# Kernel tuning notes

Measured on AMD Instinct MI355X. Metric: run time of the kernel, lower is better.

## Reference

```python
import jax, jax.numpy as jnp
import numpy as np

HEAD_DIM = 64
N_HEADS = 32
N_KV = 8
ROPE_BASE = 500000.0
FREQ_CONFIG = {"factor": 32.0, "low_freq_factor": 1.0, "high_freq_factor": 4.0, "original_context_length": 8192}


def _rope_tables(head_dim, theta, n_pos, fc):
    # faithful to precompute_rope_params with llama3 freq scaling
    inv_freq = 1.0 / theta ** (np.arange(0, head_dim, 2, dtype=np.float32) / head_dim)
    low_wl = fc["original_context_length"] / fc["low_freq_factor"]
    high_wl = fc["original_context_length"] / fc["high_freq_factor"]
    wavelen = 2.0 * np.pi / inv_freq
    inv_l = np.where(wavelen > low_wl, inv_freq / fc["factor"], inv_freq)
    smooth = (fc["original_context_length"] / wavelen - fc["low_freq_factor"]) / (fc["high_freq_factor"] - fc["low_freq_factor"])
    smoothed = (1.0 - smooth) * (inv_freq / fc["factor"]) + smooth * inv_freq
    med = (wavelen <= low_wl) & (wavelen >= high_wl)
    inv_freq = np.where(med, smoothed, inv_l)
    pos = np.arange(n_pos, dtype=np.float32)
    angles = pos[:, None] * inv_freq[None, :]          # [T, head_dim/2]
    angles = np.concatenate([angles, angles], axis=1)  # [T, head_dim]
    return jnp.asarray(np.cos(angles), jnp.float32), jnp.asarray(np.sin(angles), jnp.float32)


def _apply_rope(x, cos, sin):
    # x: [b, h, t, d]; cos/sin: [t, d]
    d = x.shape[-1]
    x1, x2 = x[..., : d // 2], x[..., d // 2:]
    rotated = jnp.concatenate([-x2, x1], axis=-1)
    return x * cos[None, None] + rotated * sin[None, None]


def setup_inputs() -> dict:
    key = jax.random.key(0)
    ks = jax.random.split(key, 5)
    b, t, d = 1, 2048, 2048
    s = 0.02
    return {
        "x": jax.random.normal(ks[0], (b, t, d), jnp.float32),
        "Wq": jax.random.normal(ks[1], (d, d), jnp.float32) * s,
        "Wk": jax.random.normal(ks[2], (N_KV * HEAD_DIM, d), jnp.float32) * s,
        "Wv": jax.random.normal(ks[3], (N_KV * HEAD_DIM, d), jnp.float32) * s,
        "Wo": jax.random.normal(ks[4], (d, d), jnp.float32) * s,
        "start_pos": 0,
    }


def reference(x, Wq, Wk, Wv, Wo, start_pos):
    b, t, _ = x.shape
    cos, sin = _rope_tables(HEAD_DIM, ROPE_BASE, start_pos + t, FREQ_CONFIG)
    cos, sin = cos[start_pos:start_pos + t], sin[start_pos:start_pos + t]

    q = (x @ Wq.T).reshape(b, t, N_HEADS, HEAD_DIM).transpose(0, 2, 1, 3)  # [b,H,t,d]
    k = (x @ Wk.T).reshape(b, t, N_KV, HEAD_DIM).transpose(0, 2, 1, 3)     # [b,G,t,d]
    v = (x @ Wv.T).reshape(b, t, N_KV, HEAD_DIM).transpose(0, 2, 1, 3)

    q = _apply_rope(q, cos, sin)
    k = _apply_rope(k, cos, sin)

    n_rep = N_HEADS // N_KV
    k = jnp.repeat(k, n_rep, axis=1)  # [b,H,t,d]
    v = jnp.repeat(v, n_rep, axis=1)

    scores = jnp.einsum("bhqd,bhkd->bhqk", q, k)
    causal = jnp.triu(jnp.ones((t, t), bool), k=1)
    scores = jnp.where(causal[None, None], -jnp.inf, scores) / jnp.sqrt(jnp.float32(HEAD_DIM))
    weights = jax.nn.softmax(scores, axis=-1)
    ctx = jnp.einsum("bhqk,bhkd->bhqd", weights, v)
    ctx = ctx.transpose(0, 2, 1, 3).reshape(b, t, N_HEADS * HEAD_DIM)
    return ctx @ Wo.T
```

## Files before the change

kernel.cpp:

```cpp
#include <hip/hip_runtime.h>
#include <math.h>

#define T_SEQ 2048
#define D_MODEL 2048
#define HEAD_DIM 64
#define N_HEADS 32
#define N_KV 8

using short8 = __attribute__((ext_vector_type(8))) short;
using f32x4  = __attribute__((ext_vector_type(4))) float;

#define MFMA16(a, b, c) __builtin_amdgcn_mfma_f32_16x16x32_bf16(a, b, c, 0, 0, 0)

__device__ __forceinline__ unsigned short f2bf(float f) {
    unsigned int u = __builtin_bit_cast(unsigned int, f);
    u += 0x7fff + ((u >> 16) & 1);
    return (unsigned short)(u >> 16);
}
__device__ __forceinline__ float bf2f(unsigned short h) {
    unsigned int u = ((unsigned int)h) << 16;
    return __builtin_bit_cast(float, u);
}
__device__ __forceinline__ void gld_lds16(const ushort* g, ushort* l) {
    __builtin_amdgcn_global_load_lds((const __attribute__((address_space(1))) void*)g,
                                     (__attribute__((address_space(3))) void*)l, 16, 0, 0);
}

__global__ void rope_tables_kernel(float* __restrict__ cosT, float* __restrict__ sinT,
                                   const int* __restrict__ start_pos, int T) {
    int t = blockIdx.x;
    int i = threadIdx.x;
    float pos = (float)(start_pos[0] + t);
    float expo = (float)i / 32.0f;
    float inv_freq = 1.0f / powf(500000.0f, expo);
    const float two_pi = 6.283185307179586f;
    float wavelen = two_pi / inv_freq;
    const float low_wl = 8192.0f;
    const float high_wl = 2048.0f;
    float inv;
    if (wavelen > low_wl) {
        inv = inv_freq / 32.0f;
    } else if (wavelen < high_wl) {
        inv = inv_freq;
    } else {
        float smooth = (8192.0f / wavelen - 1.0f) / 3.0f;
        inv = (1.0f - smooth) * (inv_freq / 32.0f) + smooth * inv_freq;
    }
    float ang = pos * inv;
    cosT[i * T + t] = cosf(ang);
    sinT[i * T + t] = sinf(ang);
}

__global__ __launch_bounds__(256) void cast_all_kernel(
    const float* __restrict__ x, const float* __restrict__ wq,
    const float* __restrict__ wk, const float* __restrict__ wv,
    const float* __restrict__ wo,
    ushort* __restrict__ xb, ushort* __restrict__ wqb,
    ushort* __restrict__ wkb, ushort* __restrict__ wvb, ushort* __restrict__ wob) {
    int i = blockIdx.x * 256 + threadIdx.x;
    const float* src; ushort* dst; int off;
    if (i < 1048576)      { src = x;  dst = xb;  off = i; }
    else if (i < 2097152) { src = wq; dst = wqb; off = i - 1048576; }
    else if (i < 2359296) { src = wk; dst = wkb; off = i - 2097152; }
    else if (i < 2621440) { src = wv; dst = wvb; off = i - 2359296; }
    else                  { src = wo; dst = wob; off = i - 2621440; }
    float4 v = ((const float4*)src)[off];
    ushort4 o;
    o.x = f2bf(v.x); o.y = f2bf(v.y); o.z = f2bf(v.z); o.w = f2bf(v.w);
    ((ushort4*)dst)[off] = o;
}

__global__ __launch_bounds__(256) void gemm_qkv(
    const ushort* __restrict__ X, const ushort* __restrict__ Wqb,
    const ushort* __restrict__ Wkb, const ushort* __restrict__ Wvb,
    ushort* __restrict__ Qo, ushort* __restrict__ Ko, ushort* __restrict__ Vto,
    const float* __restrict__ cosT, const float* __restrict__ sinT,
    int T, int D) {
    __shared__ __align__(16) ushort As[2][2048];
    __shared__ __align__(16) ushort Bs[2][4096];
    const int tid = threadIdx.x;
    const int w = tid >> 6, l = tid & 63;
    const int m0 = blockIdx.x * 64;
    const int n0g = blockIdx.y * 128;

    const ushort* B;
    ushort* Cout;
    int n0, doRope;
    if (n0g < 2048)      { B = Wqb + (size_t)n0g * D;          Cout = Qo;  n0 = n0g;        doRope = 1; }
    else if (n0g < 2560) { B = Wkb + (size_t)(n0g - 2048) * D; Cout = Ko;  n0 = n0g - 2048; doRope = 1; }
    else                 { B = Wvb + (size_t)(n0g - 2560) * D; Cout = Vto; n0 = n0g - 2560; doRope = 0; }

    const int wm = (w >> 1) * 32, wn = (w & 1) * 64;
    const int lr = l & 15;
    const int quad = l >> 4;

    f32x4 zero = {0.f, 0.f, 0.f, 0.f};
    f32x4 acc[2][4];
#pragma unroll
    for (int i = 0; i < 2; ++i)
#pragma unroll
        for (int j = 0; j < 4; ++j) acc[i][j] = zero;

    const int srow = l >> 2;
    const int scg  = ((l & 3) ^ (srow & 3)) * 8;
    const ushort* Ag0 = X + (size_t)(m0 + 16 * w + srow) * D + scg;
    const ushort* Bg0 = B + (size_t)(16 * (2 * w) + srow) * D + scg;
    const ushort* Bg1 = B + (size_t)(16 * (2 * w + 1) + srow) * D + scg;

    gld_lds16(Ag0, &As[0][w * 512]);
    gld_lds16(Bg0, &Bs[0][(2 * w) * 512]);
    gld_lds16(Bg1, &Bs[0][(2 * w + 1) * 512]);

    const int rsw = (quad ^ (lr & 3)) * 8;
    for (int k0 = 0; k0 < D; k0 += 32) {
        const int b = (k0 >> 5) & 1;
        __syncthreads();
        if (k0 + 32 < D) {
            gld_lds16(Ag0 + k0 + 32, &As[b ^ 1][w * 512]);
            gld_lds16(Bg0 + k0 + 32, &Bs[b ^ 1][(2 * w) * 512]);
            gld_lds16(Bg1 + k0 + 32, &Bs[b ^ 1][(2 * w + 1) * 512]);
        }
        short8 af[2], bf[4];
#pragma unroll
        for (int i = 0; i < 2; ++i) af[i] = *(const short8*)&As[b][(wm + i * 16 + lr) * 32 + rsw];
#pragma unroll
        for (int j = 0; j < 4; ++j) bf[j] = *(const short8*)&Bs[b][(wn + j * 16 + lr) * 32 + rsw];
#pragma unroll
        for (int i = 0; i < 2; ++i)
#pragma unroll
            for (int j = 0; j < 4; ++j)
                acc[i][j] = MFMA16(af[i], bf[j], acc[i][j]);
    }

    const int mbase = m0 + wm + quad * 4;
    if (doRope) {
#pragma unroll
        for (int i = 0; i < 2; ++i) {
            int trow = mbase + i * 16;
#pragma unroll
            for (int j = 0; j < 2; ++j) {
                int i1 = lr + j * 16;
                float4 c4 = *(const float4*)&cosT[(size_t)i1 * T + trow];
                float4 s4 = *(const float4*)&sinT[(size_t)i1 * T + trow];
                int n1 = n0 + wn + lr + j * 16;
                int n2 = n1 + 32;
                size_t b1 = (size_t)(n1 >> 6) * ((size_t)T * 64) + (size_t)(n1 & 63);
                size_t b2 = (size_t)(n2 >> 6) * ((size_t)T * 64) + (size_t)(n2 & 63);
                float cs[4] = {c4.x, c4.y, c4.z, c4.w};
                float sn[4] = {s4.x, s4.y, s4.z, s4.w};
#pragma unroll
                for (int r = 0; r < 4; ++r) {
                    float x1 = acc[i][j][r], x2 = acc[i][j + 2][r];
                    Cout[b1 + (size_t)(trow + r) * 64] = f2bf(x1 * cs[r] - x2 * sn[r]);
                    Cout[b2 + (size_t)(trow + r) * 64] = f2bf(x2 * cs[r] + x1 * sn[r]);
                }
            }
        }
    } else {
#pragma unroll
        for (int i = 0; i < 2; ++i)
#pragma unroll
            for (int j = 0; j < 4; ++j) {
                int n = n0 + wn + lr + j * 16;
                int m = mbase + i * 16;
                ushort4 o;
                o.x = f2bf(acc[i][j][0]); o.y = f2bf(acc[i][j][1]);
                o.z = f2bf(acc[i][j][2]); o.w = f2bf(acc[i][j][3]);
                *(ushort4*)&Vto[(size_t)n * T + m] = o;
            }
    }
}

__global__ __launch_bounds__(256) void gemm_bt_f32(const ushort* __restrict__ A,
                                                   const ushort* __restrict__ B,
                                                   float* __restrict__ C,
                                                   int M, int N, int K) {
    __shared__ __align__(16) ushort As[2][2048];
    __shared__ __align__(16) ushort Bs[2][4096];
    const int tid = threadIdx.x;
    const int w = tid >> 6, l = tid & 63;
    const int m0 = blockIdx.x * 64, n0 = blockIdx.y * 128;
    const int wm = (w >> 1) * 32, wn = (w & 1) * 64;
    const int lr = l & 15;
    const int quad = l >> 4;

    f32x4 zero = {0.f, 0.f, 0.f, 0.f};
    f32x4 acc[2][4];
#pragma unroll
    for (int i = 0; i < 2; ++i)
#pragma unroll
        for (int j = 0; j < 4; ++j) acc[i][j] = zero;

    const int srow = l >> 2;
    const int scg  = ((l & 3) ^ (srow & 3)) * 8;
    const ushort* Ag0 = A + (size_t)(m0 + 16 * w + srow) * K + scg;
    const ushort* Bg0 = B + (size_t)(n0 + 16 * (2 * w) + srow) * K + scg;
    const ushort* Bg1 = B + (size_t)(n0 + 16 * (2 * w + 1) + srow) * K + scg;

    gld_lds16(Ag0, &As[0][w * 512]);
    gld_lds16(Bg0, &Bs[0][(2 * w) * 512]);
    gld_lds16(Bg1, &Bs[0][(2 * w + 1) * 512]);

    const int rsw = (quad ^ (lr & 3)) * 8;
    for (int k0 = 0; k0 < K; k0 += 32) {
        const int b = (k0 >> 5) & 1;
        __syncthreads();
        if (k0 + 32 < K) {
            gld_lds16(Ag0 + k0 + 32, &As[b ^ 1][w * 512]);
            gld_lds16(Bg0 + k0 + 32, &Bs[b ^ 1][(2 * w) * 512]);
            gld_lds16(Bg1 + k0 + 32, &Bs[b ^ 1][(2 * w + 1) * 512]);
        }
        short8 af[2], bf[4];
#pragma unroll
        for (int i = 0; i < 2; ++i) af[i] = *(const short8*)&As[b][(wm + i * 16 + lr) * 32 + rsw];
#pragma unroll
        for (int j = 0; j < 4; ++j) bf[j] = *(const short8*)&Bs[b][(wn + j * 16 + lr) * 32 + rsw];
#pragma unroll
        for (int i = 0; i < 2; ++i)
#pragma unroll
            for (int j = 0; j < 4; ++j)
                acc[i][j] = MFMA16(af[i], bf[j], acc[i][j]);
    }

    const int mbase = m0 + wm + quad * 4;
    const int nbase = n0 + wn + lr;
#pragma unroll
    for (int i = 0; i < 2; ++i)
#pragma unroll
        for (int j = 0; j < 4; ++j)
#pragma unroll
            for (int r = 0; r < 4; ++r)
                C[(size_t)(mbase + i * 16 + r) * N + (nbase + j * 16)] = acc[i][j][r];
}

__global__ __launch_bounds__(256) void attn_mfma(const ushort* __restrict__ Q,
                                                 const ushort* __restrict__ K,
                                                 const ushort* __restrict__ Vt,
                                                 ushort* __restrict__ ctx, int T) {
    __shared__ __align__(16) ushort Ks[2][4096];
    __shared__ __align__(16) ushort Vs[2][4096];
    __shared__ __align__(16) ushort Ps[4][2304];
    const int tid = threadIdx.x, w = tid >> 6, l = tid & 63;
    const int lr = l & 15, quad = l >> 4;
    const int h = blockIdx.y, hk = h >> 2;
    const ushort* Kb = K + (size_t)hk * T * 64;
    const ushort* Vb = Vt + (size_t)hk * 64 * T;

    const int srow = l >> 3;
    const int sc   = ((l & 7) ^ srow) * 8;
    const int si0 = 2 * w, si1 = 2 * w + 1;
    const int swz = (lr & 7);
    f32x4 zero = {0.f, 0.f, 0.f, 0.f};

    for (int phase = 0; phase < 2; ++phase) {
        const int qt = phase == 0 ? (15 - (int)blockIdx.x) : (int)blockIdx.x;
        const int qbase = qt * 128;

        short8 qf[2][2];
#pragma unroll
        for (int ni = 0; ni < 2; ++ni)
#pragma unroll
            for (int ks = 0; ks < 2; ++ks)
                qf[ni][ks] = *(const short8*)(Q + ((size_t)h * T + qbase + w * 32 + ni * 16 + lr) * 64 + ks * 32 + quad * 8);

        f32x4 oacc[2][4];
#pragma unroll
        for (int ni = 0; ni < 2; ++ni)
#pragma unroll
            for (int dj = 0; dj < 4; ++dj) oacc[ni][dj] = zero;
        float lsum[2] = {0.f, 0.f};

        const int ntiles = 2 * qt + 2;
        const int diag = 2 * qt + (w >> 1);
        const int qrow0 = qbase + w * 32 + lr;

        gld_lds16(Kb + (size_t)(8 * si0 + srow) * 64 + sc, &Ks[0][si0 * 512]);
        gld_lds16(Kb + (size_t)(8 * si1 + srow) * 64 + sc, &Ks[0][si1 * 512]);
        gld_lds16(Vb + (size_t)(8 * si0 + srow) * T + sc, &Vs[0][si0 * 512]);
        gld_lds16(Vb + (size_t)(8 * si1 + srow) * T + sc, &Vs[0][si1 * 512]);

        for (int kt = 0; kt < ntiles; ++kt) {
            const int b = kt & 1;
            __syncthreads();
            if (kt + 1 < ntiles) {
                const int k0n = (kt + 1) * 64;
                gld_lds16(Kb + (size_t)(k0n + 8 * si0 + srow) * 64 + sc, &Ks[b ^ 1][si0 * 512]);
                gld_lds16(Kb + (size_t)(k0n + 8 * si1 + srow) * 64 + sc, &Ks[b ^ 1][si1 * 512]);
                gld_lds16(Vb + (size_t)(8 * si0 + srow) * T + k0n + sc, &Vs[b ^ 1][si0 * 512]);
                gld_lds16(Vb + (size_t)(8 * si1 + srow) * T + k0n + sc, &Vs[b ^ 1][si1 * 512]);
            }
            if (kt > diag) continue;
            const int k0 = kt * 64;

            f32x4 s[4][2];
#pragma unroll
            for (int mi = 0; mi < 4; ++mi)
#pragma unroll
                for (int ni = 0; ni < 2; ++ni) s[mi][ni] = zero;
#pragma unroll
            for (int ks = 0; ks < 2; ++ks)
#pragma unroll
                for (int mi = 0; mi < 4; ++mi) {
                    short8 kf = *(const short8*)&Ks[b][(mi * 16 + lr) * 64 + ((4 * ks + quad) ^ swz) * 8];
                    s[mi][0] = MFMA16(kf, qf[0][ks], s[mi][0]);
                    s[mi][1] = MFMA16(kf, qf[1][ks], s[mi][1]);
                }

            const bool masked = (kt == diag);
#pragma unroll
            for (int mi = 0; mi < 4; ++mi)
#pragma unroll
                for (int ni = 0; ni < 2; ++ni) {
                    float pv[4];
#pragma unroll
                    for (int r = 0; r < 4; ++r) {
                        float p = __expf(s[mi][ni][r] * 0.125f);
                        if (masked && (k0 + mi * 16 + quad * 4 + r > qrow0 + ni * 16)) p = 0.f;
                        lsum[ni] += p;
                        pv[r] = p;
                    }
                    ushort4 pk;
                    pk.x = f2bf(pv[0]); pk.y = f2bf(pv[1]); pk.z = f2bf(pv[2]); pk.w = f2bf(pv[3]);
                    *(ushort4*)&Ps[w][(ni * 16 + lr) * 72 + mi * 16 + quad * 4] = pk;
                }

#pragma unroll
            for (int ks2 = 0; ks2 < 2; ++ks2) {
                short8 pf0 = *(const short8*)&Ps[w][lr * 72 + ks2 * 32 + quad * 8];
                short8 pf1 = *(const short8*)&Ps[w][(16 + lr) * 72 + ks2 * 32 + quad * 8];
#pragma unroll
                for (int dj = 0; dj < 4; ++dj) {
                    short8 vf = *(const short8*)&Vs[b][(dj * 16 + lr) * 64 + ((4 * ks2 + quad) ^ swz) * 8];
                    oacc[0][dj] = MFMA16(pf0, vf, oacc[0][dj]);
                    oacc[1][dj] = MFMA16(pf1, vf, oacc[1][dj]);
                }
            }
        }

        float inv[2][4];
#pragma unroll
        for (int ni = 0; ni < 2; ++ni) {
            float v = lsum[ni];
            v += __shfl_xor(v, 16, 64);
            v += __shfl_xor(v, 32, 64);
#pragma unroll
            for (int r = 0; r < 4; ++r)
                inv[ni][r] = 1.f / __shfl(v, quad * 4 + r, 64);
        }

#pragma unroll
        for (int ni = 0; ni < 2; ++ni)
#pragma unroll
            for (int dj = 0; dj < 4; ++dj) {
                int col = h * 64 + dj * 16 + lr;
#pragma unroll
                for (int r = 0; r < 4; ++r) {
                    int row = qbase + w * 32 + ni * 16 + quad * 4 + r;
                    ctx[(size_t)row * 2048 + col] = f2bf(oacc[ni][dj][r] * inv[ni][r]);
                }
            }
    }
}

extern "C" void kernel_launch(void* const* d_in, const int* in_sizes, int n_in,
                              void* d_out, int out_size, void* d_ws, size_t ws_size,
                              hipStream_t stream) {
    const float* x  = (const float*)d_in[0];
    const float* Wq = (const float*)d_in[1];
    const float* Wk = (const float*)d_in[2];
    const float* Wv = (const float*)d_in[3];
    const float* Wo = (const float*)d_in[4];
    const int* start_pos = (const int*)d_in[5];
    float* out = (float*)d_out;

    const int T = T_SEQ, D = D_MODEL;
    const int KV = N_KV * HEAD_DIM;

    char* w = (char*)d_ws;
    float* cosT = (float*)w;            w += (size_t)32 * T * 4;
    float* sinT = (float*)w;            w += (size_t)32 * T * 4;
    ushort* xbf  = (ushort*)w;          w += (size_t)T * D * 2;
    ushort* wqbf = (ushort*)w;          w += (size_t)D * D * 2;
    ushort* wkbf = (ushort*)w;          w += (size_t)KV * D * 2;
    ushort* wvbf = (ushort*)w;          w += (size_t)KV * D * 2;
    ushort* wobf = (ushort*)w;          w += (size_t)D * D * 2;
    ushort* qbf  = (ushort*)w;          w += (size_t)N_HEADS * T * 64 * 2;
    ushort* kbf  = (ushort*)w;          w += (size_t)N_KV * T * 64 * 2;
    ushort* vtbf = (ushort*)w;          w += (size_t)N_KV * 64 * T * 2;
    ushort* ctxbf = xbf;

    rope_tables_kernel<<<dim3(T), dim3(32), 0, stream>>>(cosT, sinT, start_pos, T);

    cast_all_kernel<<<dim3(14336), dim3(256), 0, stream>>>(x, Wq, Wk, Wv, Wo,
                                                           xbf, wqbf, wkbf, wvbf, wobf);

    gemm_qkv<<<dim3(T / 64, (D + 2 * KV) / 128), dim3(256), 0, stream>>>(
        xbf, wqbf, wkbf, wvbf, qbf, kbf, vtbf, cosT, sinT, T, D);

    attn_mfma<<<dim3(8, N_HEADS), dim3(256), 0, stream>>>(qbf, kbf, vtbf, ctxbf, T);

    gemm_bt_f32<<<dim3(T / 64, D / 128), dim3(256), 0, stream>>>(ctxbf, wobf, out, T, D, D);
}
```

Before: 251.5 us.

## Split attention key range across two warp groups and deepen GEMM K-stage

The attention kernel now runs 512 threads per block. Two groups of four warps each process alternate 64-key tiles for the same query rows, and their partial outputs and row sums are merged through shared memory at the end of each phase. Both GEMM kernels now stage 64 K-columns per iteration instead of 32, which halves the number of barriers and loop trips. The cost is more shared memory per block, an extra merge step with added barriers, and possible loss of occupancy.

Result: faster. 218.6 us (-13.1%).

```diff
diff --git a/kernel.cpp b/kernel.cpp
--- a/kernel.cpp
+++ b/kernel.cpp
@@ -16,10 +16,6 @@
     unsigned int u = __builtin_bit_cast(unsigned int, f);
     u += 0x7fff + ((u >> 16) & 1);
     return (unsigned short)(u >> 16);
-}
-__device__ __forceinline__ float bf2f(unsigned short h) {
-    unsigned int u = ((unsigned int)h) << 16;
-    return __builtin_bit_cast(float, u);
 }
 __device__ __forceinline__ void gld_lds16(const ushort* g, ushort* l) {
     __builtin_amdgcn_global_load_lds((const __attribute__((address_space(1))) void*)g,
@@ -76,8 +72,8 @@
     ushort* __restrict__ Qo, ushort* __restrict__ Ko, ushort* __restrict__ Vto,
     const float* __restrict__ cosT, const float* __restrict__ sinT,
     int T, int D) {
-    __shared__ __align__(16) ushort As[2][2048];
-    __shared__ __align__(16) ushort Bs[2][4096];
+    __shared__ __align__(16) ushort As[2][2][2048];
+    __shared__ __align__(16) ushort Bs[2][2][4096];
     const int tid = threadIdx.x;
     const int w = tid >> 6, l = tid & 63;
     const int m0 = blockIdx.x * 64;
@@ -103,34 +99,40 @@
 
     const int srow = l >> 2;
     const int scg  = ((l & 3) ^ (srow & 3)) * 8;
-    const ushort* Ag0 = X + (size_t)(m0 + 16 * w + srow) * D + scg;
+    const ushort* Ag  = X + (size_t)(m0 + 16 * w + srow) * D + scg;
     const ushort* Bg0 = B + (size_t)(16 * (2 * w) + srow) * D + scg;
     const ushort* Bg1 = B + (size_t)(16 * (2 * w + 1) + srow) * D + scg;
 
-    gld_lds16(Ag0, &As[0][w * 512]);
-    gld_lds16(Bg0, &Bs[0][(2 * w) * 512]);
-    gld_lds16(Bg1, &Bs[0][(2 * w + 1) * 512]);
+#define GSTAGE(k0v, nb) { \
+    gld_lds16(Ag  + (k0v),      &As[nb][0][w * 512]); \
+    gld_lds16(Ag  + (k0v) + 32, &As[nb][1][w * 512]); \
+    gld_lds16(Bg0 + (k0v),      &Bs[nb][0][(2 * w) * 512]); \
+    gld_lds16(Bg0 + (k0v) + 32, &Bs[nb][1][(2 * w) * 512]); \
+    gld_lds16(Bg1 + (k0v),      &Bs[nb][0][(2 * w + 1) * 512]); \
+    gld_lds16(Bg1 + (k0v) + 32, &Bs[nb][1][(2 * w + 1) * 512]); }
+
+    GSTAGE(0, 0);
 
     const int rsw = (quad ^ (lr & 3)) * 8;
-    for (int k0 = 0; k0 < D; k0 += 32) {
-        const int b = (k0 >> 5) & 1;
+    for (int k0 = 0; k0 < D; k0 += 64) {
+        const int b = (k0 >> 6) & 1;
         __syncthreads();
-        if (k0 + 32 < D) {
-            gld_lds16(Ag0 + k0 + 32, &As[b ^ 1][w * 512]);
-            gld_lds16(Bg0 + k0 + 32, &Bs[b ^ 1][(2 * w) * 512]);
-            gld_lds16(Bg1 + k0 + 32, &Bs[b ^ 1][(2 * w + 1) * 512]);
-        }
-        short8 af[2], bf[4];
-#pragma unroll
-        for (int i = 0; i < 2; ++i) af[i] = *(const short8*)&As[b][(wm + i * 16 + lr) * 32 + rsw];
-#pragma unroll
-        for (int j = 0; j < 4; ++j) bf[j] = *(const short8*)&Bs[b][(wn + j * 16 + lr) * 32 + rsw];
-#pragma unroll
-        for (int i = 0; i < 2; ++i)
-#pragma unroll
-            for (int j = 0; j < 4; ++j)
-                acc[i][j] = MFMA16(af[i], bf[j], acc[i][j]);
+        if (k0 + 64 < D) GSTAGE(k0 + 64, b ^ 1);
+#pragma unroll
+        for (int sub = 0; sub < 2; ++sub) {
+            short8 af[2], bf[4];
+#pragma unroll
+            for (int i = 0; i < 2; ++i) af[i] = *(const short8*)&As[b][sub][(wm + i * 16 + lr) * 32 + rsw];
+#pragma unroll
+            for (int j = 0; j < 4; ++j) bf[j] = *(const short8*)&Bs[b][sub][(wn + j * 16 + lr) * 32 + rsw];
+#pragma unroll
+            for (int i = 0; i < 2; ++i)
+#pragma unroll
+                for (int j = 0; j < 4; ++j)
+                    acc[i][j] = MFMA16(af[i], bf[j], acc[i][j]);
+        }
     }
+#undef GSTAGE
 
     const int mbase = m0 + wm + quad * 4;
     if (doRope) {
@@ -175,8 +177,8 @@
                                                    const ushort* __restrict__ B,
                                                    float* __restrict__ C,
                                                    int M, int N, int K) {
-    __shared__ __align__(16) ushort As[2][2048];
-    __shared__ __align__(16) ushort Bs[2][4096];
+    __shared__ __align__(16) ushort As[2][2][2048];
+    __shared__ __align__(16) ushort Bs[2][2][4096];
     const int tid = threadIdx.x;
     const int w = tid >> 6, l = tid & 63;
     const int m0 = blockIdx.x * 64, n0 = blockIdx.y * 128;
@@ -193,34 +195,40 @@
 
     const int srow = l >> 2;
     const int scg  = ((l & 3) ^ (srow & 3)) * 8;
-    const ushort* Ag0 = A + (size_t)(m0 + 16 * w + srow) * K + scg;
+    const ushort* Ag  = A + (size_t)(m0 + 16 * w + srow) * K + scg;
     const ushort* Bg0 = B + (size_t)(n0 + 16 * (2 * w) + srow) * K + scg;
     const ushort* Bg1 = B + (size_t)(n0 + 16 * (2 * w + 1) + srow) * K + scg;
 
-    gld_lds16(Ag0, &As[0][w * 512]);
-    gld_lds16(Bg0, &Bs[0][(2 * w) * 512]);
-    gld_lds16(Bg1, &Bs[0][(2 * w + 1) * 512]);
+#define GSTAGE(k0v, nb) { \
+    gld_lds16(Ag  + (k0v),      &As[nb][0][w * 512]); \
+    gld_lds16(Ag  + (k0v) + 32, &As[nb][1][w * 512]); \
+    gld_lds16(Bg0 + (k0v),      &Bs[nb][0][(2 * w) * 512]); \
+    gld_lds16(Bg0 + (k0v) + 32, &Bs[nb][1][(2 * w) * 512]); \
+    gld_lds16(Bg1 + (k0v),      &Bs[nb][0][(2 * w + 1) * 512]); \
+    gld_lds16(Bg1 + (k0v) + 32, &Bs[nb][1][(2 * w + 1) * 512]); }
+
+    GSTAGE(0, 0);
 
     const int rsw = (quad ^ (lr & 3)) * 8;
-    for (int k0 = 0; k0 < K; k0 += 32) {
-        const int b = (k0 >> 5) & 1;
+    for (int k0 = 0; k0 < K; k0 += 64) {
+        const int b = (k0 >> 6) & 1;
         __syncthreads();
-        if (k0 + 32 < K) {
-            gld_lds16(Ag0 + k0 + 32, &As[b ^ 1][w * 512]);
-            gld_lds16(Bg0 + k0 + 32, &Bs[b ^ 1][(2 * w) * 512]);
-            gld_lds16(Bg1 + k0 + 32, &Bs[b ^ 1][(2 * w + 1) * 512]);
-        }
-        short8 af[2], bf[4];
-#pragma unroll
-        for (int i = 0; i < 2; ++i) af[i] = *(const short8*)&As[b][(wm + i * 16 + lr) * 32 + rsw];
-#pragma unroll
-        for (int j = 0; j < 4; ++j) bf[j] = *(const short8*)&Bs[b][(wn + j * 16 + lr) * 32 + rsw];
-#pragma unroll
-        for (int i = 0; i < 2; ++i)
-#pragma unroll
-            for (int j = 0; j < 4; ++j)
-                acc[i][j] = MFMA16(af[i], bf[j], acc[i][j]);
+        if (k0 + 64 < K) GSTAGE(k0 + 64, b ^ 1);
+#pragma unroll
+        for (int sub = 0; sub < 2; ++sub) {
+            short8 af[2], bf[4];
+#pragma unroll
+            for (int i = 0; i < 2; ++i) af[i] = *(const short8*)&As[b][sub][(wm + i * 16 + lr) * 32 + rsw];
+#pragma unroll
+            for (int j = 0; j < 4; ++j) bf[j] = *(const short8*)&Bs[b][sub][(wn + j * 16 + lr) * 32 + rsw];
+#pragma unroll
+            for (int i = 0; i < 2; ++i)
+#pragma unroll
+                for (int j = 0; j < 4; ++j)
+                    acc[i][j] = MFMA16(af[i], bf[j], acc[i][j]);
+        }
     }
+#undef GSTAGE
 
     const int mbase = m0 + wm + quad * 4;
     const int nbase = n0 + wn + lr;
@@ -233,14 +241,18 @@
                 C[(size_t)(mbase + i * 16 + r) * N + (nbase + j * 16)] = acc[i][j][r];
 }
 
-__global__ __launch_bounds__(256) void attn_mfma(const ushort* __restrict__ Q,
+__global__ __launch_bounds__(512) void attn_mfma(const ushort* __restrict__ Q,
                                                  const ushort* __restrict__ K,
                                                  const ushort* __restrict__ Vt,
                                                  ushort* __restrict__ ctx, int T) {
-    __shared__ __align__(16) ushort Ks[2][4096];
-    __shared__ __align__(16) ushort Vs[2][4096];
-    __shared__ __align__(16) ushort Ps[4][2304];
+    __shared__ __align__(16) ushort Ks[2][2][4096];
+    __shared__ __align__(16) ushort Vs[2][2][4096];
+    __shared__ __align__(16) ushort Ps[8][2304];
+    float* mrg = (float*)&Ps[0][0];
+
     const int tid = threadIdx.x, w = tid >> 6, l = tid & 63;
+    const int pw = w >> 2;
+    const int rg = w & 3;
     const int lr = l & 15, quad = l >> 4;
     const int h = blockIdx.y, hk = h >> 2;
     const ushort* Kb = K + (size_t)hk * T * 64;
@@ -248,20 +260,36 @@
 
     const int srow = l >> 3;
     const int sc   = ((l & 7) ^ srow) * 8;
-    const int si0 = 2 * w, si1 = 2 * w + 1;
-    const int swz = (lr & 7);
+    const int swz  = lr & 7;
+    const int tw = w >> 1;
+    const int half4 = (w & 1) * 4;
     f32x4 zero = {0.f, 0.f, 0.f, 0.f};
+
+#define ASTAGE(ss, nb) { \
+    const int ke_ = (ss) * 128; \
+    _Pragma("unroll") \
+    for (int i_ = 0; i_ < 4; ++i_) { \
+        const int segq_ = half4 + i_; \
+        const int grow_ = segq_ * 8 + srow; \
+        if (tw == 0)      gld_lds16(Kb + (size_t)(ke_ + grow_) * 64 + sc,      &Ks[nb][0][segq_ * 512]); \
+        else if (tw == 1) gld_lds16(Kb + (size_t)(ke_ + 64 + grow_) * 64 + sc, &Ks[nb][1][segq_ * 512]); \
+        else if (tw == 2) gld_lds16(Vb + (size_t)grow_ * T + ke_ + sc,         &Vs[nb][0][segq_ * 512]); \
+        else              gld_lds16(Vb + (size_t)grow_ * T + ke_ + 64 + sc,    &Vs[nb][1][segq_ * 512]); \
+    } }
 
     for (int phase = 0; phase < 2; ++phase) {
         const int qt = phase == 0 ? (15 - (int)blockIdx.x) : (int)blockIdx.x;
         const int qbase = qt * 128;
+        const int diag_rg = 2 * qt + (rg >> 1);
+        const int qrow0 = qbase + rg * 32 + lr;
+        const int nst = qt + 1;
 
         short8 qf[2][2];
 #pragma unroll
         for (int ni = 0; ni < 2; ++ni)
 #pragma unroll
             for (int ks = 0; ks < 2; ++ks)
-                qf[ni][ks] = *(const short8*)(Q + ((size_t)h * T + qbase + w * 32 + ni * 16 + lr) * 64 + ks * 32 + quad * 8);
+                qf[ni][ks] = *(const short8*)(Q + ((size_t)h * T + qbase + rg * 32 + ni * 16 + lr) * 64 + ks * 32 + quad * 8);
 
         f32x4 oacc[2][4];
 #pragma unroll
@@ -270,96 +298,115 @@
             for (int dj = 0; dj < 4; ++dj) oacc[ni][dj] = zero;
         float lsum[2] = {0.f, 0.f};
 
-        const int ntiles = 2 * qt + 2;
-        const int diag = 2 * qt + (w >> 1);
-        const int qrow0 = qbase + w * 32 + lr;
-
-        gld_lds16(Kb + (size_t)(8 * si0 + srow) * 64 + sc, &Ks[0][si0 * 512]);
-        gld_lds16(Kb + (size_t)(8 * si1 + srow) * 64 + sc, &Ks[0][si1 * 512]);
-        gld_lds16(Vb + (size_t)(8 * si0 + srow) * T + sc, &Vs[0][si0 * 512]);
-        gld_lds16(Vb + (size_t)(8 * si1 + srow) * T + sc, &Vs[0][si1 * 512]);
-
-        for (int kt = 0; kt < ntiles; ++kt) {
-            const int b = kt & 1;
+        ASTAGE(0, 0);
+
+        for (int st = 0; st < nst; ++st) {
+            const int b = st & 1;
             __syncthreads();
-            if (kt + 1 < ntiles) {
-                const int k0n = (kt + 1) * 64;
-                gld_lds16(Kb + (size_t)(k0n + 8 * si0 + srow) * 64 + sc, &Ks[b ^ 1][si0 * 512]);
-                gld_lds16(Kb + (size_t)(k0n + 8 * si1 + srow) * 64 + sc, &Ks[b ^ 1][si1 * 512]);
-                gld_lds16(Vb + (size_t)(8 * si0 + srow) * T + k0n + sc, &Vs[b ^ 1][si0 * 512]);
-                gld_lds16(Vb + (size_t)(8 * si1 + srow) * T + k0n + sc, &Vs[b ^ 1][si1 * 512]);
-            }
-            if (kt > diag) continue;
-            const int k0 = kt * 64;
-
-            f32x4 s[4][2];
-#pragma unroll
-            for (int mi = 0; mi < 4; ++mi)
-#pragma unroll
-                for (int ni = 0; ni < 2; ++ni) s[mi][ni] = zero;
-#pragma unroll
-            for (int ks = 0; ks < 2; ++ks)
-#pragma unroll
-                for (int mi = 0; mi < 4; ++mi) {
-                    short8 kf = *(const short8*)&Ks[b][(mi * 16 + lr) * 64 + ((4 * ks + quad) ^ swz) * 8];
-                    s[mi][0] = MFMA16(kf, qf[0][ks], s[mi][0]);
-                    s[mi][1] = MFMA16(kf, qf[1][ks], s[mi][1]);
-                }
-
-            const bool masked = (kt == diag);
-#pragma unroll
-            for (int mi = 0; mi < 4; ++mi)
-#pragma unroll
-                for (int ni = 0; ni < 2; ++ni) {
-                    float pv[4];
-#pragma unroll
-                    for (int r = 0; r < 4; ++r) {
-                        float p = __expf(s[mi][ni][r] * 0.125f);
-                        if (masked && (k0 + mi * 16 + quad * 4 + r > qrow0 + ni * 16)) p = 0.f;
-                        lsum[ni] += p;
-                        pv[r] = p;
+            if (st + 1 < nst) ASTAGE(st + 1, b ^ 1);
+
+            const int kt = 2 * st + pw;
+            if (kt <= diag_rg) {
+                const int k0 = kt * 64;
+                const ushort* KsB = &Ks[b][pw][0];
+                const ushort* VsB = &Vs[b][pw][0];
+
+                f32x4 s[4][2];
+#pragma unroll
+                for (int mi = 0; mi < 4; ++mi)
+#pragma unroll
+                    for (int ni = 0; ni < 2; ++ni) s[mi][ni] = zero;
+#pragma unroll
+                for (int ks = 0; ks < 2; ++ks)
+#pragma unroll
+                    for (int mi = 0; mi < 4; ++mi) {
+                        short8 kf = *(const short8*)&KsB[(mi * 16 + lr) * 64 + ((4 * ks + quad) ^ swz) * 8];
+                        s[mi][0] = MFMA16(kf, qf[0][ks], s[mi][0]);
+                        s[mi][1] = MFMA16(kf, qf[1][ks], s[mi][1]);
                     }
-                    ushort4 pk;
-                    pk.x = f2bf(pv[0]); pk.y = f2bf(pv[1]); pk.z = f2bf(pv[2]); pk.w = f2bf(pv[3]);
-                    *(ushort4*)&Ps[w][(ni * 16 + lr) * 72 + mi * 16 + quad * 4] = pk;
-                }
-
-#pragma unroll
-            for (int ks2 = 0; ks2 < 2; ++ks2) {
-                short8 pf0 = *(const short8*)&Ps[w][lr * 72 + ks2 * 32 + quad * 8];
-                short8 pf1 = *(const short8*)&Ps[w][(16 + lr) * 72 + ks2 * 32 + quad * 8];
-#pragma unroll
-                for (int dj = 0; dj < 4; ++dj) {
-                    short8 vf = *(const short8*)&Vs[b][(dj * 16 + lr) * 64 + ((4 * ks2 + quad) ^ swz) * 8];
-                    oacc[0][dj] = MFMA16(pf0, vf, oacc[0][dj]);
-                    oacc[1][dj] = MFMA16(pf1, vf, oacc[1][dj]);
+
+                const bool masked = (kt == diag_rg);
+#pragma unroll
+                for (int mi = 0; mi < 4; ++mi)
+#pragma unroll
+                    for (int ni = 0; ni < 2; ++ni) {
+                        float pv[4];
+#pragma unroll
+                        for (int r = 0; r < 4; ++r) {
+                            float p = __expf(s[mi][ni][r] * 0.125f);
+                            if (masked && (k0 + mi * 16 + quad * 4 + r > qrow0 + ni * 16)) p = 0.f;
+                            lsum[ni] += p;
+                            pv[r] = p;
+                        }
+                        ushort4 pk;
+                        pk.x = f2bf(pv[0]); pk.y = f2bf(pv[1]); pk.z = f2bf(pv[2]); pk.w = f2bf(pv[3]);
+                        *(ushort4*)&Ps[w][(ni * 16 + lr) * 72 + mi * 16 + quad * 4] = pk;
+                    }
+
+#pragma unroll
+                for (int ks2 = 0; ks2 < 2; ++ks2) {
+                    short8 pf0 = *(const short8*)&Ps[w][lr * 72 + ks2 * 32 + quad * 8];
+                    short8 pf1 = *(const short8*)&Ps[w][(16 + lr) * 72 + ks2 * 32 + quad * 8];
+#pragma unroll
+                    for (int dj = 0; dj < 4; ++dj) {
+                        short8 vf = *(const short8*)&VsB[(dj * 16 + lr) * 64 + ((4 * ks2 + quad) ^ swz) * 8];
+                        oacc[0][dj] = MFMA16(pf0, vf, oacc[0][dj]);
+                        oacc[1][dj] = MFMA16(pf1, vf, oacc[1][dj]);
+                    }
                 }
             }
         }
 
-        float inv[2][4];
+        float vred[2];
 #pragma unroll
         for (int ni = 0; ni < 2; ++ni) {
             float v = lsum[ni];
             v += __shfl_xor(v, 16, 64);
             v += __shfl_xor(v, 32, 64);
-#pragma unroll
-            for (int r = 0; r < 4; ++r)
-                inv[ni][r] = 1.f / __shfl(v, quad * 4 + r, 64);
-        }
-
-#pragma unroll
-        for (int ni = 0; ni < 2; ++ni)
-#pragma unroll
-            for (int dj = 0; dj < 4; ++dj) {
-                int col = h * 64 + dj * 16 + lr;
-#pragma unroll
-                for (int r = 0; r < 4; ++r) {
-                    int row = qbase + w * 32 + ni * 16 + quad * 4 + r;
-                    ctx[(size_t)row * 2048 + col] = f2bf(oacc[ni][dj][r] * inv[ni][r]);
+            vred[ni] = v;
+        }
+
+        __syncthreads();
+        if (pw == 1) {
+#pragma unroll
+            for (int ni = 0; ni < 2; ++ni)
+#pragma unroll
+                for (int dj = 0; dj < 4; ++dj)
+#pragma unroll
+                    for (int r = 0; r < 4; ++r)
+                        mrg[rg * 2048 + ((ni * 4 + dj) * 4 + r) * 64 + l] = oacc[ni][dj][r];
+            if (quad == 0) {
+#pragma unroll
+                for (int ni = 0; ni < 2; ++ni)
+                    mrg[8192 + rg * 32 + ni * 16 + lr] = vred[ni];
+            }
+        }
+        __syncthreads();
+        if (pw == 0) {
+            float inv[2][4];
+#pragma unroll
+            for (int ni = 0; ni < 2; ++ni) {
+                float vtot = vred[ni] + mrg[8192 + rg * 32 + ni * 16 + lr];
+#pragma unroll
+                for (int r = 0; r < 4; ++r)
+                    inv[ni][r] = 1.f / __shfl(vtot, quad * 4 + r, 64);
+            }
+#pragma unroll
+            for (int ni = 0; ni < 2; ++ni)
+#pragma unroll
+                for (int dj = 0; dj < 4; ++dj) {
+                    int col = h * 64 + dj * 16 + lr;
+#pragma unroll
+                    for (int r = 0; r < 4; ++r) {
+                        float o = oacc[ni][dj][r] + mrg[rg * 2048 + ((ni * 4 + dj) * 4 + r) * 64 + l];
+                        int row = qbase + rg * 32 + ni * 16 + quad * 4 + r;
+                        ctx[(size_t)row * 2048 + col] = f2bf(o * inv[ni][r]);
+                    }
                 }
-            }
+        }
+        __syncthreads();
     }
+#undef ASTAGE
 }
 
 extern "C" void kernel_launch(void* const* d_in, const int* in_sizes, int n_in,
@@ -397,7 +444,7 @@
     gemm_qkv<<<dim3(T / 64, (D + 2 * KV) / 128), dim3(256), 0, stream>>>(
         xbf, wqbf, wkbf, wvbf, qbf, kbf, vtbf, cosT, sinT, T, D);
 
-    attn_mfma<<<dim3(8, N_HEADS), dim3(256), 0, stream>>>(qbf, kbf, vtbf, ctxbf, T);
+    attn_mfma<<<dim3(8, N_HEADS), dim3(512), 0, stream>>>(qbf, kbf, vtbf, ctxbf, T);
 
     gemm_bt_f32<<<dim3(T / 64, D / 128), dim3(256), 0, stream>>>(ctxbf, wobf, out, T, D, D);
 }
```

## Deepen GEMM K-stage to 64 and shrink attention query tiles to 64 rows

Applied to the files above, without the earlier changes.

Both GEMM kernels now stage 64 K-columns per barrier (two 32-wide sub-tiles per buffer), which halves the number of __syncthreads and loop iterations at the cost of double the LDS per block. The attention kernel switches from 128-row query tiles over an 8-block grid to 64-row tiles over a 16-block grid, with each wave owning 16 query rows. Work is still paired across two phases for causal load balance, and a barrier is added between phases. This raises parallelism across CUs and removes the per-wave skip logic, but reloads K/V tiles for twice as many query tiles.

Result: faster. 213.0 us (-15.3%).

```diff
diff --git a/kernel.cpp b/kernel.cpp
--- a/kernel.cpp
+++ b/kernel.cpp
@@ -16,10 +16,6 @@
     unsigned int u = __builtin_bit_cast(unsigned int, f);
     u += 0x7fff + ((u >> 16) & 1);
     return (unsigned short)(u >> 16);
-}
-__device__ __forceinline__ float bf2f(unsigned short h) {
-    unsigned int u = ((unsigned int)h) << 16;
-    return __builtin_bit_cast(float, u);
 }
 __device__ __forceinline__ void gld_lds16(const ushort* g, ushort* l) {
     __builtin_amdgcn_global_load_lds((const __attribute__((address_space(1))) void*)g,
@@ -76,8 +72,8 @@
     ushort* __restrict__ Qo, ushort* __restrict__ Ko, ushort* __restrict__ Vto,
     const float* __restrict__ cosT, const float* __restrict__ sinT,
     int T, int D) {
-    __shared__ __align__(16) ushort As[2][2048];
-    __shared__ __align__(16) ushort Bs[2][4096];
+    __shared__ __align__(16) ushort As[2][2][2048];
+    __shared__ __align__(16) ushort Bs[2][2][4096];
     const int tid = threadIdx.x;
     const int w = tid >> 6, l = tid & 63;
     const int m0 = blockIdx.x * 64;
@@ -103,34 +99,40 @@
 
     const int srow = l >> 2;
     const int scg  = ((l & 3) ^ (srow & 3)) * 8;
-    const ushort* Ag0 = X + (size_t)(m0 + 16 * w + srow) * D + scg;
+    const ushort* Ag  = X + (size_t)(m0 + 16 * w + srow) * D + scg;
     const ushort* Bg0 = B + (size_t)(16 * (2 * w) + srow) * D + scg;
     const ushort* Bg1 = B + (size_t)(16 * (2 * w + 1) + srow) * D + scg;
 
-    gld_lds16(Ag0, &As[0][w * 512]);
-    gld_lds16(Bg0, &Bs[0][(2 * w) * 512]);
-    gld_lds16(Bg1, &Bs[0][(2 * w + 1) * 512]);
+#define GSTAGE(k0v, nb) { \
+    gld_lds16(Ag  + (k0v),      &As[nb][0][w * 512]); \
+    gld_lds16(Ag  + (k0v) + 32, &As[nb][1][w * 512]); \
+    gld_lds16(Bg0 + (k0v),      &Bs[nb][0][(2 * w) * 512]); \
+    gld_lds16(Bg0 + (k0v) + 32, &Bs[nb][1][(2 * w) * 512]); \
+    gld_lds16(Bg1 + (k0v),      &Bs[nb][0][(2 * w + 1) * 512]); \
+    gld_lds16(Bg1 + (k0v) + 32, &Bs[nb][1][(2 * w + 1) * 512]); }
+
+    GSTAGE(0, 0);
 
     const int rsw = (quad ^ (lr & 3)) * 8;
-    for (int k0 = 0; k0 < D; k0 += 32) {
-        const int b = (k0 >> 5) & 1;
+    for (int k0 = 0; k0 < D; k0 += 64) {
+        const int b = (k0 >> 6) & 1;
         __syncthreads();
-        if (k0 + 32 < D) {
-            gld_lds16(Ag0 + k0 + 32, &As[b ^ 1][w * 512]);
-            gld_lds16(Bg0 + k0 + 32, &Bs[b ^ 1][(2 * w) * 512]);
-            gld_lds16(Bg1 + k0 + 32, &Bs[b ^ 1][(2 * w + 1) * 512]);
-        }
-        short8 af[2], bf[4];
-#pragma unroll
-        for (int i = 0; i < 2; ++i) af[i] = *(const short8*)&As[b][(wm + i * 16 + lr) * 32 + rsw];
-#pragma unroll
-        for (int j = 0; j < 4; ++j) bf[j] = *(const short8*)&Bs[b][(wn + j * 16 + lr) * 32 + rsw];
-#pragma unroll
-        for (int i = 0; i < 2; ++i)
-#pragma unroll
-            for (int j = 0; j < 4; ++j)
-                acc[i][j] = MFMA16(af[i], bf[j], acc[i][j]);
-    }
+        if (k0 + 64 < D) GSTAGE(k0 + 64, b ^ 1);
+#pragma unroll
+        for (int sub = 0; sub < 2; ++sub) {
+            short8 af[2], bf[4];
+#pragma unroll
+            for (int i = 0; i < 2; ++i) af[i] = *(const short8*)&As[b][sub][(wm + i * 16 + lr) * 32 + rsw];
+#pragma unroll
+            for (int j = 0; j < 4; ++j) bf[j] = *(const short8*)&Bs[b][sub][(wn + j * 16 + lr) * 32 + rsw];
+#pragma unroll
+            for (int i = 0; i < 2; ++i)
+#pragma unroll
+                for (int j = 0; j < 4; ++j)
+                    acc[i][j] = MFMA16(af[i], bf[j], acc[i][j]);
+        }
+    }
+#undef GSTAGE
 
     const int mbase = m0 + wm + quad * 4;
     if (doRope) {
@@ -175,8 +177,8 @@
                                                    const ushort* __restrict__ B,
                                                    float* __restrict__ C,
                                                    int M, int N, int K) {
-    __shared__ __align__(16) ushort As[2][2048];
-    __shared__ __align__(16) ushort Bs[2][4096];
+    __shared__ __align__(16) ushort As[2][2][2048];
+    __shared__ __align__(16) ushort Bs[2][2][4096];
     const int tid = threadIdx.x;
     const int w = tid >> 6, l = tid & 63;
     const int m0 = blockIdx.x * 64, n0 = blockIdx.y * 128;
@@ -193,34 +195,40 @@
 
     const int srow = l >> 2;
     const int scg  = ((l & 3) ^ (srow & 3)) * 8;
-    const ushort* Ag0 = A + (size_t)(m0 + 16 * w + srow) * K + scg;
+    const ushort* Ag  = A + (size_t)(m0 + 16 * w + srow) * K + scg;
     const ushort* Bg0 = B + (size_t)(n0 + 16 * (2 * w) + srow) * K + scg;
     const ushort* Bg1 = B + (size_t)(n0 + 16 * (2 * w + 1) + srow) * K + scg;
 
-    gld_lds16(Ag0, &As[0][w * 512]);
-    gld_lds16(Bg0, &Bs[0][(2 * w) * 512]);
-    gld_lds16(Bg1, &Bs[0][(2 * w + 1) * 512]);
+#define GSTAGE(k0v, nb) { \
+    gld_lds16(Ag  + (k0v),      &As[nb][0][w * 512]); \
+    gld_lds16(Ag  + (k0v) + 32, &As[nb][1][w * 512]); \
+    gld_lds16(Bg0 + (k0v),      &Bs[nb][0][(2 * w) * 512]); \
+    gld_lds16(Bg0 + (k0v) + 32, &Bs[nb][1][(2 * w) * 512]); \
+    gld_lds16(Bg1 + (k0v),      &Bs[nb][0][(2 * w + 1) * 512]); \
+    gld_lds16(Bg1 + (k0v) + 32, &Bs[nb][1][(2 * w + 1) * 512]); }
+
+    GSTAGE(0, 0);
 
     const int rsw = (quad ^ (lr & 3)) * 8;
-    for (int k0 = 0; k0 < K; k0 += 32) {
-        const int b = (k0 >> 5) & 1;
+    for (int k0 = 0; k0 < K; k0 += 64) {
+        const int b = (k0 >> 6) & 1;
         __syncthreads();
-        if (k0 + 32 < K) {
-            gld_lds16(Ag0 + k0 + 32, &As[b ^ 1][w * 512]);
-            gld_lds16(Bg0 + k0 + 32, &Bs[b ^ 1][(2 * w) * 512]);
-            gld_lds16(Bg1 + k0 + 32, &Bs[b ^ 1][(2 * w + 1) * 512]);
-        }
-        short8 af[2], bf[4];
-#pragma unroll
-        for (int i = 0; i < 2; ++i) af[i] = *(const short8*)&As[b][(wm + i * 16 + lr) * 32 + rsw];
-#pragma unroll
-        for (int j = 0; j < 4; ++j) bf[j] = *(const short8*)&Bs[b][(wn + j * 16 + lr) * 32 + rsw];
-#pragma unroll
-        for (int i = 0; i < 2; ++i)
-#pragma unroll
-            for (int j = 0; j < 4; ++j)
-                acc[i][j] = MFMA16(af[i], bf[j], acc[i][j]);
-    }
+        if (k0 + 64 < K) GSTAGE(k0 + 64, b ^ 1);
+#pragma unroll
+        for (int sub = 0; sub < 2; ++sub) {
+            short8 af[2], bf[4];
+#pragma unroll
+            for (int i = 0; i < 2; ++i) af[i] = *(const short8*)&As[b][sub][(wm + i * 16 + lr) * 32 + rsw];
+#pragma unroll
+            for (int j = 0; j < 4; ++j) bf[j] = *(const short8*)&Bs[b][sub][(wn + j * 16 + lr) * 32 + rsw];
+#pragma unroll
+            for (int i = 0; i < 2; ++i)
+#pragma unroll
+                for (int j = 0; j < 4; ++j)
+                    acc[i][j] = MFMA16(af[i], bf[j], acc[i][j]);
+        }
+    }
+#undef GSTAGE
 
     const int mbase = m0 + wm + quad * 4;
     const int nbase = n0 + wn + lr;
@@ -239,7 +247,7 @@
                                                  ushort* __restrict__ ctx, int T) {
     __shared__ __align__(16) ushort Ks[2][4096];
     __shared__ __align__(16) ushort Vs[2][4096];
-    __shared__ __align__(16) ushort Ps[4][2304];
+    __shared__ __align__(16) ushort Ps[4][1152];
     const int tid = threadIdx.x, w = tid >> 6, l = tid & 63;
     const int lr = l & 15, quad = l >> 4;
     const int h = blockIdx.y, hk = h >> 2;
@@ -249,30 +257,24 @@
     const int srow = l >> 3;
     const int sc   = ((l & 7) ^ srow) * 8;
     const int si0 = 2 * w, si1 = 2 * w + 1;
-    const int swz = (lr & 7);
+    const int swz = lr & 7;
     f32x4 zero = {0.f, 0.f, 0.f, 0.f};
 
     for (int phase = 0; phase < 2; ++phase) {
-        const int qt = phase == 0 ? (15 - (int)blockIdx.x) : (int)blockIdx.x;
-        const int qbase = qt * 128;
-
-        short8 qf[2][2];
-#pragma unroll
-        for (int ni = 0; ni < 2; ++ni)
-#pragma unroll
-            for (int ks = 0; ks < 2; ++ks)
-                qf[ni][ks] = *(const short8*)(Q + ((size_t)h * T + qbase + w * 32 + ni * 16 + lr) * 64 + ks * 32 + quad * 8);
-
-        f32x4 oacc[2][4];
-#pragma unroll
-        for (int ni = 0; ni < 2; ++ni)
-#pragma unroll
-            for (int dj = 0; dj < 4; ++dj) oacc[ni][dj] = zero;
-        float lsum[2] = {0.f, 0.f};
-
-        const int ntiles = 2 * qt + 2;
-        const int diag = 2 * qt + (w >> 1);
-        const int qrow0 = qbase + w * 32 + lr;
+        const int qt = phase == 0 ? (31 - (int)blockIdx.x) : (int)blockIdx.x;
+        const int qbase = qt * 64;
+        const int qrow_abs = qbase + w * 16 + lr;
+        const int ntiles = qt + 1;
+
+        short8 qf[2];
+#pragma unroll
+        for (int ks = 0; ks < 2; ++ks)
+            qf[ks] = *(const short8*)(Q + ((size_t)h * T + qbase + w * 16 + lr) * 64 + ks * 32 + quad * 8);
+
+        f32x4 oacc[4];
+#pragma unroll
+        for (int dj = 0; dj < 4; ++dj) oacc[dj] = zero;
+        float lsum = 0.f;
 
         gld_lds16(Kb + (size_t)(8 * si0 + srow) * 64 + sc, &Ks[0][si0 * 512]);
         gld_lds16(Kb + (size_t)(8 * si1 + srow) * 64 + sc, &Ks[0][si1 * 512]);
@@ -289,76 +291,64 @@
                 gld_lds16(Vb + (size_t)(8 * si0 + srow) * T + k0n + sc, &Vs[b ^ 1][si0 * 512]);
                 gld_lds16(Vb + (size_t)(8 * si1 + srow) * T + k0n + sc, &Vs[b ^ 1][si1 * 512]);
             }
-            if (kt > diag) continue;
             const int k0 = kt * 64;
 
-            f32x4 s[4][2];
-#pragma unroll
-            for (int mi = 0; mi < 4; ++mi)
-#pragma unroll
-                for (int ni = 0; ni < 2; ++ni) s[mi][ni] = zero;
+            f32x4 s[4];
+#pragma unroll
+            for (int mi = 0; mi < 4; ++mi) s[mi] = zero;
 #pragma unroll
             for (int ks = 0; ks < 2; ++ks)
 #pragma unroll
                 for (int mi = 0; mi < 4; ++mi) {
                     short8 kf = *(const short8*)&Ks[b][(mi * 16 + lr) * 64 + ((4 * ks + quad) ^ swz) * 8];
-                    s[mi][0] = MFMA16(kf, qf[0][ks], s[mi][0]);
-                    s[mi][1] = MFMA16(kf, qf[1][ks], s[mi][1]);
+                    s[mi] = MFMA16(kf, qf[ks], s[mi]);
                 }
 
-            const bool masked = (kt == diag);
-#pragma unroll
-            for (int mi = 0; mi < 4; ++mi)
-#pragma unroll
-                for (int ni = 0; ni < 2; ++ni) {
-                    float pv[4];
-#pragma unroll
-                    for (int r = 0; r < 4; ++r) {
-                        float p = __expf(s[mi][ni][r] * 0.125f);
-                        if (masked && (k0 + mi * 16 + quad * 4 + r > qrow0 + ni * 16)) p = 0.f;
-                        lsum[ni] += p;
-                        pv[r] = p;
-                    }
-                    ushort4 pk;
-                    pk.x = f2bf(pv[0]); pk.y = f2bf(pv[1]); pk.z = f2bf(pv[2]); pk.w = f2bf(pv[3]);
-                    *(ushort4*)&Ps[w][(ni * 16 + lr) * 72 + mi * 16 + quad * 4] = pk;
+            const bool masked = (kt == qt);
+#pragma unroll
+            for (int mi = 0; mi < 4; ++mi) {
+                float pv[4];
+#pragma unroll
+                for (int r = 0; r < 4; ++r) {
+                    float p = __expf(s[mi][r] * 0.125f);
+                    if (masked && (k0 + mi * 16 + quad * 4 + r > qrow_abs)) p = 0.f;
+                    lsum += p;
+                    pv[r] = p;
                 }
+                ushort4 pk;
+                pk.x = f2bf(pv[0]); pk.y = f2bf(pv[1]); pk.z = f2bf(pv[2]); pk.w = f2bf(pv[3]);
+                *(ushort4*)&Ps[w][lr * 72 + mi * 16 + quad * 4] = pk;
+            }
 
 #pragma unroll
             for (int ks2 = 0; ks2 < 2; ++ks2) {
-                short8 pf0 = *(const short8*)&Ps[w][lr * 72 + ks2 * 32 + quad * 8];
-                short8 pf1 = *(const short8*)&Ps[w][(16 + lr) * 72 + ks2 * 32 + quad * 8];
+                short8 pf = *(const short8*)&Ps[w][lr * 72 + ks2 * 32 + quad * 8];
 #pragma unroll
                 for (int dj = 0; dj < 4; ++dj) {
                     short8 vf = *(const short8*)&Vs[b][(dj * 16 + lr) * 64 + ((4 * ks2 + quad) ^ swz) * 8];
-                    oacc[0][dj] = MFMA16(pf0, vf, oacc[0][dj]);
-                    oacc[1][dj] = MFMA16(pf1, vf, oacc[1][dj]);
+                    oacc[dj] = MFMA16(pf, vf, oacc[dj]);
                 }
             }
         }
 
-        float inv[2][4];
-#pragma unroll
-        for (int ni = 0; ni < 2; ++ni) {
-            float v = lsum[ni];
-            v += __shfl_xor(v, 16, 64);
-            v += __shfl_xor(v, 32, 64);
-#pragma unroll
-            for (int r = 0; r < 4; ++r)
-                inv[ni][r] = 1.f / __shfl(v, quad * 4 + r, 64);
-        }
-
-#pragma unroll
-        for (int ni = 0; ni < 2; ++ni)
-#pragma unroll
-            for (int dj = 0; dj < 4; ++dj) {
-                int col = h * 64 + dj * 16 + lr;
-#pragma unroll
-                for (int r = 0; r < 4; ++r) {
-                    int row = qbase + w * 32 + ni * 16 + quad * 4 + r;
-                    ctx[(size_t)row * 2048 + col] = f2bf(oacc[ni][dj][r] * inv[ni][r]);
-                }
-            }
+        float v = lsum;
+        v += __shfl_xor(v, 16, 64);
+        v += __shfl_xor(v, 32, 64);
+        float invr[4];
+#pragma unroll
+        for (int r = 0; r < 4; ++r)
+            invr[r] = 1.f / __shfl(v, quad * 4 + r, 64);
+
+#pragma unroll
+        for (int dj = 0; dj < 4; ++dj) {
+            int col = h * 64 + dj * 16 + lr;
+#pragma unroll
+            for (int r = 0; r < 4; ++r) {
+                int row = qbase + w * 16 + quad * 4 + r;
+                ctx[(size_t)row * 2048 + col] = f2bf(oacc[dj][r] * invr[r]);
+            }
+        }
+        __syncthreads();
     }
 }
 
@@ -397,7 +387,7 @@
     gemm_qkv<<<dim3(T / 64, (D + 2 * KV) / 128), dim3(256), 0, stream>>>(
         xbf, wqbf, wkbf, wvbf, qbf, kbf, vtbf, cosT, sinT, T, D);
 
-    attn_mfma<<<dim3(8, N_HEADS), dim3(256), 0, stream>>>(qbf, kbf, vtbf, ctxbf, T);
+    attn_mfma<<<dim3(16, N_HEADS), dim3(256), 0, stream>>>(qbf, kbf, vtbf, ctxbf, T);
 
     gemm_bt_f32<<<dim3(T / 64, D / 128), dim3(256), 0, stream>>>(ctxbf, wobf, out, T, D, D);
 }
```
